# Performance work log

Measured on AMD Instinct MI355X. Metric: run time of the kernel, lower is better.

The kernel has to match this reference:

```python
import jax, jax.numpy as jnp
import numpy as np

S, B, H = 1024, 8, 1024   # seq (num_tokens//WORLD_SIZE), batch, hidden
T = S * B                 # total tokens
E, K, F = 8, 2, 4096      # experts, top_k, ffn hidden (4*H)


def setup_inputs() -> dict:
    key = jax.random.key(0)
    k0, k1, k2, k3, k4 = jax.random.split(key, 5)
    hidden_states = jax.random.normal(k0, (S, B, H), dtype=jnp.float32)
    # precomputed top-k router probs (normalized like softmax top-k output)
    gw = jax.random.uniform(k1, (T, K), dtype=jnp.float32) + 1e-3
    gate_weight = gw / jnp.sum(gw, axis=-1, keepdims=True)
    choosed_experts = jax.random.randint(k2, (T, K), 0, E).astype(jnp.int64)
    w1 = jax.random.normal(k3, (E, H, F), dtype=jnp.float32) * 0.02
    w2 = jax.random.normal(k4, (E, F, H), dtype=jnp.float32) * 0.02
    return {"hidden_states": hidden_states, "gate_weight": gate_weight,
            "choosed_experts": choosed_experts, "w1": w1, "w2": w2}


def reference(hidden_states, gate_weight, choosed_experts, w1, w2):
    # Megatron MoE with precomputed routing: dispatch tokens to top-k experts,
    # per-expert MLP (fc1 -> gelu -> fc2, no bias), combine weighted by probs.
    x = hidden_states.reshape(-1, H)  # [T, H]
    n_exp = w1.shape[0]
    # coef[t, e] = sum_k gate_weight[t, k] * 1[choosed_experts[t, k] == e]
    onehot = jax.nn.one_hot(choosed_experts, n_exp, dtype=gate_weight.dtype)  # [T, K, E]
    coef = jnp.einsum('tk,tke->te', gate_weight, onehot)  # [T, E]
    out = jnp.zeros_like(x)
    for e in range(n_exp):  # fixed small loop over experts (grouped GEMM)
        h = jax.nn.gelu(x @ w1[e])          # [T, F]
        out = out + coef[:, e:e + 1] * (h @ w2[e])  # [T, H]
    output = out.reshape(-1, H)
    return output  # mlp_bias is None in grouped-GEMM Megatron experts
```

## Files before the change

### kernel.cpp

```cpp
#include <hip/hip_runtime.h>
#include <stdint.h>

#define T 8192
#define H 1024
#define F 4096
#define E 8
#define K_TOP 2
#define TK (T * K_TOP)

#define BM 128
#define BN 128
#define BK 32

typedef unsigned short u16;
typedef __bf16 bf16x8 __attribute__((ext_vector_type(8)));
typedef float f32x4 __attribute__((ext_vector_type(4)));

__device__ __forceinline__ u16 f2bf(float f) {
    union { float f; uint32_t u; } v; v.f = f;
    uint32_t r = v.u + 0x7FFFu + ((v.u >> 16) & 1u);
    return (u16)(r >> 16);
}

__device__ __forceinline__ void async_cp16(const u16* g, u16* l) {
    __builtin_amdgcn_global_load_lds(
        (const __attribute__((address_space(1))) void*)g,
        (__attribute__((address_space(3))) void*)l, 16, 0, 0);
}

__global__ __launch_bounds__(256) void count_kernel(const int* __restrict__ ce,
                                                    int* __restrict__ counts) {
    int p = blockIdx.x * 256 + threadIdx.x;
    if (p < TK) atomicAdd(&counts[ce[p]], 1);
}

__global__ void scan_kernel(const int* __restrict__ counts, int* __restrict__ offsets) {
    if (threadIdx.x == 0) {
        int s = 0;
        for (int e = 0; e < E; e++) { offsets[e] = s; s += counts[e]; }
    }
}

__global__ __launch_bounds__(256) void fill_kernel(const int* __restrict__ ce,
                                                   const float* __restrict__ gate,
                                                   const int* __restrict__ offsets,
                                                   int* __restrict__ fill,
                                                   int* __restrict__ tokbuf,
                                                   float* __restrict__ gwbuf) {
    int p = blockIdx.x * 256 + threadIdx.x;
    if (p < TK) {
        int e = ce[p];
        int pos = offsets[e] + atomicAdd(&fill[e], 1);
        tokbuf[pos] = p >> 1;
        gwbuf[pos] = gate[p];
    }
}

__global__ __launch_bounds__(256) void cvt_bf16(const float* __restrict__ in,
                                                u16* __restrict__ out, int n) {
    int i = (blockIdx.x * 256 + threadIdx.x) * 4;
    if (i < n) {
        float4 v = *(const float4*)(in + i);
        ushort4 o;
        o.x = f2bf(v.x); o.y = f2bf(v.y); o.z = f2bf(v.z); o.w = f2bf(v.w);
        *(ushort4*)(out + i) = o;
    }
}

__global__ __launch_bounds__(256) void transpose_cvt(const float* __restrict__ in,
                                                     u16* __restrict__ out,
                                                     int R, int C) {
    __shared__ u16 tile[64][66];
    int e = blockIdx.z;
    const float* src = in + (size_t)e * R * C;
    u16* dst = out + (size_t)e * R * C;
    int c0 = blockIdx.x * 64, r0 = blockIdx.y * 64;
    int tx = threadIdx.x & 63, ty = threadIdx.x >> 6;
#pragma unroll
    for (int p = 0; p < 16; p++) {
        int row = ty + p * 4;
        tile[row][tx] = f2bf(src[(size_t)(r0 + row) * C + c0 + tx]);
    }
    __syncthreads();
#pragma unroll
    for (int p = 0; p < 16; p++) {
        int row = ty + p * 4;
        dst[(size_t)(c0 + row) * R + r0 + tx] = tile[tx][row];
    }
}

__global__ __launch_bounds__(256, 2) void fc1_kernel(const u16* __restrict__ xb,
                                                     const u16* __restrict__ w1t,
                                                     const int* __restrict__ tokbuf,
                                                     const int* __restrict__ counts,
                                                     const int* __restrict__ offsets,
                                                     u16* __restrict__ hbuf) {
    __shared__ __align__(16) u16 As[BM * BK];
    __shared__ __align__(16) u16 Bs[BN * BK];

    const int e = blockIdx.z;
    const int cnt = counts[e];
    const int off = offsets[e];
    const int nt = blockIdx.x;
    const int tid = threadIdx.x;
    const int lane = tid & 63;
    const int wave = tid >> 6;
    const int wr = wave >> 1, wc = wave & 1;
    const int quad = lane >> 4, l16 = lane & 15;
    const int r0 = tid >> 2;
    const int kc = tid & 3;

    for (int rt = blockIdx.y; rt * BM < cnt; rt += gridDim.y) {
        int m0 = rt * BM + r0, m1 = m0 + 64;
        int t0 = tokbuf[off + (m0 < cnt ? m0 : cnt - 1)];
        int t1 = tokbuf[off + (m1 < cnt ? m1 : cnt - 1)];
        const u16* a0 = xb + (size_t)t0 * H + kc * 8;
        const u16* a1 = xb + (size_t)t1 * H + kc * 8;
        const u16* b0 = w1t + ((size_t)e * F + nt * BN + r0) * H + kc * 8;
        const u16* b1 = b0 + (size_t)64 * H;

        f32x4 acc[4][4];
#pragma unroll
        for (int i = 0; i < 4; i++)
#pragma unroll
            for (int j = 0; j < 4; j++) acc[i][j] = (f32x4)0.f;

        for (int k0 = 0; k0 < H; k0 += BK) {
            __syncthreads();
            async_cp16(a0 + k0, &As[tid * 8]);
            async_cp16(a1 + k0, &As[(tid + 256) * 8]);
            async_cp16(b0 + k0, &Bs[tid * 8]);
            async_cp16(b1 + k0, &Bs[(tid + 256) * 8]);
            __syncthreads();

            bf16x8 af[4], bfv[4];
#pragma unroll
            for (int mi = 0; mi < 4; mi++)
                af[mi] = *(const bf16x8*)&As[(wr * 64 + mi * 16 + l16) * BK + quad * 8];
#pragma unroll
            for (int ni = 0; ni < 4; ni++)
                bfv[ni] = *(const bf16x8*)&Bs[(wc * 64 + ni * 16 + l16) * BK + quad * 8];
#pragma unroll
            for (int mi = 0; mi < 4; mi++)
#pragma unroll
                for (int ni = 0; ni < 4; ni++)
                    acc[mi][ni] = __builtin_amdgcn_mfma_f32_16x16x32_bf16(
                        af[mi], bfv[ni], acc[mi][ni], 0, 0, 0);
        }

#pragma unroll
        for (int mi = 0; mi < 4; mi++) {
#pragma unroll
            for (int r = 0; r < 4; r++) {
                int m = rt * BM + wr * 64 + mi * 16 + quad * 4 + r;
                if (m < cnt) {
                    size_t rowbase = (size_t)(off + m) * F;
#pragma unroll
                    for (int ni = 0; ni < 4; ni++) {
                        float v = acc[mi][ni][r];
                        float u = 0.7978845608028654f * (v + 0.044715f * v * v * v);
                        float g = v / (1.f + __expf(-2.f * u));
                        int fcol = nt * BN + wc * 64 + ni * 16 + l16;
                        hbuf[rowbase + fcol] = f2bf(g);
                    }
                }
            }
        }
    }
}

__global__ __launch_bounds__(256, 2) void fc2_kernel(const u16* __restrict__ hbuf,
                                                     const u16* __restrict__ w2t,
                                                     const int* __restrict__ tokbuf,
                                                     const float* __restrict__ gwbuf,
                                                     const int* __restrict__ counts,
                                                     const int* __restrict__ offsets,
                                                     float* __restrict__ out) {
    __shared__ __align__(16) u16 As[BM * BK];
    __shared__ __align__(16) u16 Bs[BN * BK];

    const int e = blockIdx.z;
    const int cnt = counts[e];
    const int off = offsets[e];
    const int nt = blockIdx.x;
    const int tid = threadIdx.x;
    const int lane = tid & 63;
    const int wave = tid >> 6;
    const int wr = wave >> 1, wc = wave & 1;
    const int quad = lane >> 4, l16 = lane & 15;
    const int r0 = tid >> 2;
    const int kc = tid & 3;

    for (int rt = blockIdx.y; rt * BM < cnt; rt += gridDim.y) {
        int m0 = rt * BM + r0, m1 = m0 + 64;
        int s0 = off + (m0 < cnt ? m0 : cnt - 1);
        int s1 = off + (m1 < cnt ? m1 : cnt - 1);
        const u16* a0 = hbuf + (size_t)s0 * F + kc * 8;
        const u16* a1 = hbuf + (size_t)s1 * F + kc * 8;
        const u16* b0 = w2t + ((size_t)e * H + nt * BN + r0) * F + kc * 8;
        const u16* b1 = b0 + (size_t)64 * F;

        f32x4 acc[4][4];
#pragma unroll
        for (int i = 0; i < 4; i++)
#pragma unroll
            for (int j = 0; j < 4; j++) acc[i][j] = (f32x4)0.f;

        for (int k0 = 0; k0 < F; k0 += BK) {
            __syncthreads();
            async_cp16(a0 + k0, &As[tid * 8]);
            async_cp16(a1 + k0, &As[(tid + 256) * 8]);
            async_cp16(b0 + k0, &Bs[tid * 8]);
            async_cp16(b1 + k0, &Bs[(tid + 256) * 8]);
            __syncthreads();

            bf16x8 af[4], bfv[4];
#pragma unroll
            for (int mi = 0; mi < 4; mi++)
                af[mi] = *(const bf16x8*)&As[(wr * 64 + mi * 16 + l16) * BK + quad * 8];
#pragma unroll
            for (int ni = 0; ni < 4; ni++)
                bfv[ni] = *(const bf16x8*)&Bs[(wc * 64 + ni * 16 + l16) * BK + quad * 8];
#pragma unroll
            for (int mi = 0; mi < 4; mi++)
#pragma unroll
                for (int ni = 0; ni < 4; ni++)
                    acc[mi][ni] = __builtin_amdgcn_mfma_f32_16x16x32_bf16(
                        af[mi], bfv[ni], acc[mi][ni], 0, 0, 0);
        }

#pragma unroll
        for (int mi = 0; mi < 4; mi++) {
#pragma unroll
            for (int r = 0; r < 4; r++) {
                int m = rt * BM + wr * 64 + mi * 16 + quad * 4 + r;
                if (m < cnt) {
                    int t = tokbuf[off + m];
                    float g = gwbuf[off + m];
                    size_t obase = (size_t)t * H;
#pragma unroll
                    for (int ni = 0; ni < 4; ni++) {
                        int col = nt * BN + wc * 64 + ni * 16 + l16;
                        atomicAdd(&out[obase + col], g * acc[mi][ni][r]);
                    }
                }
            }
        }
    }
}

extern "C" void kernel_launch(void* const* d_in, const int* in_sizes, int n_in,
                              void* d_out, int out_size, void* d_ws, size_t ws_size,
                              hipStream_t stream) {
    const float* x    = (const float*)d_in[0];
    const float* gate = (const float*)d_in[1];
    const int*   ce   = (const int*)d_in[2];
    const float* w1   = (const float*)d_in[3];
    const float* w2   = (const float*)d_in[4];
    float* out = (float*)d_out;
    char* ws = (char*)d_ws;

    int*   counts  = (int*)(ws + 0);
    int*   fill    = (int*)(ws + 32);
    int*   offsets = (int*)(ws + 64);
    int*   tokbuf  = (int*)(ws + 256);
    float* gwbuf   = (float*)(ws + 256 + TK * 4);
    size_t o = 256 + (size_t)TK * 8;
    u16* xb  = (u16*)(ws + o);  o += (size_t)T * H * 2;
    u16* w1t = (u16*)(ws + o);  o += (size_t)E * F * H * 2;
    u16* w2t = (u16*)(ws + o);  o += (size_t)E * H * F * 2;
    u16* hbuf = (u16*)(ws + o);

    hipMemsetAsync(ws, 0, 256, stream);
    hipMemsetAsync(d_out, 0, (size_t)T * H * sizeof(float), stream);

    count_kernel<<<TK / 256, 256, 0, stream>>>(ce, counts);
    scan_kernel<<<1, 64, 0, stream>>>(counts, offsets);
    fill_kernel<<<TK / 256, 256, 0, stream>>>(ce, gate, offsets, fill, tokbuf, gwbuf);

    cvt_bf16<<<(T * H) / (256 * 4), 256, 0, stream>>>(x, xb, T * H);
    transpose_cvt<<<dim3(F / 64, H / 64, E), 256, 0, stream>>>(w1, w1t, H, F);
    transpose_cvt<<<dim3(H / 64, F / 64, E), 256, 0, stream>>>(w2, w2t, F, H);

    fc1_kernel<<<dim3(F / BN, 32, E), 256, 0, stream>>>(xb, w1t, tokbuf, counts, offsets, hbuf);
    fc2_kernel<<<dim3(H / BN, 32, E), 256, 0, stream>>>(hbuf, w2t, tokbuf, gwbuf, counts, offsets, out);
}
```

Before: 934.3 us.

## Double-buffer LDS tiles in expert GEMMs and vectorize weight transpose

Both grouped GEMM kernels now keep two LDS buffers per operand and issue the async copy for the next K-slice before running the MFMAs on the current one. This cuts the loop to one barrier per iteration and lets global loads overlap with compute. The weight transpose-convert kernel now reads float4 and writes ushort4 instead of scalars. LDS use per block doubles, which may lower occupancy. Whether the async copy has finished before the single barrier depends on how async_cp16 waits.

```diff
diff --git a/kernel.cpp b/kernel.cpp
--- a/kernel.cpp
+++ b/kernel.cpp
@@ -75,17 +75,27 @@
     const float* src = in + (size_t)e * R * C;
     u16* dst = out + (size_t)e * R * C;
     int c0 = blockIdx.x * 64, r0 = blockIdx.y * 64;
-    int tx = threadIdx.x & 63, ty = threadIdx.x >> 6;
-#pragma unroll
-    for (int p = 0; p < 16; p++) {
-        int row = ty + p * 4;
-        tile[row][tx] = f2bf(src[(size_t)(r0 + row) * C + c0 + tx]);
+    int q = threadIdx.x & 15;
+    int s = threadIdx.x >> 4;
+#pragma unroll
+    for (int p = 0; p < 4; p++) {
+        int row = s + p * 16;
+        float4 v = *(const float4*)(src + (size_t)(r0 + row) * C + c0 + q * 4);
+        tile[row][q * 4 + 0] = f2bf(v.x);
+        tile[row][q * 4 + 1] = f2bf(v.y);
+        tile[row][q * 4 + 2] = f2bf(v.z);
+        tile[row][q * 4 + 3] = f2bf(v.w);
     }
     __syncthreads();
 #pragma unroll
-    for (int p = 0; p < 16; p++) {
-        int row = ty + p * 4;
-        dst[(size_t)(c0 + row) * R + r0 + tx] = tile[tx][row];
+    for (int p = 0; p < 4; p++) {
+        int c = s + p * 16;
+        ushort4 o;
+        o.x = tile[q * 4 + 0][c];
+        o.y = tile[q * 4 + 1][c];
+        o.z = tile[q * 4 + 2][c];
+        o.w = tile[q * 4 + 3][c];
+        *(ushort4*)(dst + (size_t)(c0 + c) * R + r0 + q * 4) = o;
     }
 }
 
@@ -95,8 +105,8 @@
                                                      const int* __restrict__ counts,
                                                      const int* __restrict__ offsets,
                                                      u16* __restrict__ hbuf) {
-    __shared__ __align__(16) u16 As[BM * BK];
-    __shared__ __align__(16) u16 Bs[BN * BK];
+    __shared__ __align__(16) u16 As[2][BM * BK];
+    __shared__ __align__(16) u16 Bs[2][BM * BK];
 
     const int e = blockIdx.z;
     const int cnt = counts[e];
@@ -125,27 +135,38 @@
 #pragma unroll
             for (int j = 0; j < 4; j++) acc[i][j] = (f32x4)0.f;
 
+        async_cp16(a0, &As[0][tid * 8]);
+        async_cp16(a1, &As[0][(tid + 256) * 8]);
+        async_cp16(b0, &Bs[0][tid * 8]);
+        async_cp16(b1, &Bs[0][(tid + 256) * 8]);
+        __syncthreads();
+
+        int cur = 0;
         for (int k0 = 0; k0 < H; k0 += BK) {
-            __syncthreads();
-            async_cp16(a0 + k0, &As[tid * 8]);
-            async_cp16(a1 + k0, &As[(tid + 256) * 8]);
-            async_cp16(b0 + k0, &Bs[tid * 8]);
-            async_cp16(b1 + k0, &Bs[(tid + 256) * 8]);
-            __syncthreads();
+            int kn = k0 + BK;
+            if (kn < H) {
+                async_cp16(a0 + kn, &As[cur ^ 1][tid * 8]);
+                async_cp16(a1 + kn, &As[cur ^ 1][(tid + 256) * 8]);
+                async_cp16(b0 + kn, &Bs[cur ^ 1][tid * 8]);
+                async_cp16(b1 + kn, &Bs[cur ^ 1][(tid + 256) * 8]);
+            }
 
             bf16x8 af[4], bfv[4];
 #pragma unroll
             for (int mi = 0; mi < 4; mi++)
-                af[mi] = *(const bf16x8*)&As[(wr * 64 + mi * 16 + l16) * BK + quad * 8];
+                af[mi] = *(const bf16x8*)&As[cur][(wr * 64 + mi * 16 + l16) * BK + quad * 8];
 #pragma unroll
             for (int ni = 0; ni < 4; ni++)
-                bfv[ni] = *(const bf16x8*)&Bs[(wc * 64 + ni * 16 + l16) * BK + quad * 8];
+                bfv[ni] = *(const bf16x8*)&Bs[cur][(wc * 64 + ni * 16 + l16) * BK + quad * 8];
 #pragma unroll
             for (int mi = 0; mi < 4; mi++)
 #pragma unroll
                 for (int ni = 0; ni < 4; ni++)
                     acc[mi][ni] = __builtin_amdgcn_mfma_f32_16x16x32_bf16(
                         af[mi], bfv[ni], acc[mi][ni], 0, 0, 0);
+
+            __syncthreads();
+            cur ^= 1;
         }
 
 #pragma unroll
@@ -176,8 +197,8 @@
                                                      const int* __restrict__ counts,
                                                      const int* __restrict__ offsets,
                                                      float* __restrict__ out) {
-    __shared__ __align__(16) u16 As[BM * BK];
-    __shared__ __align__(16) u16 Bs[BN * BK];
+    __shared__ __align__(16) u16 As[2][BM * BK];
+    __shared__ __align__(16) u16 Bs[2][BM * BK];
 
     const int e = blockIdx.z;
     const int cnt = counts[e];
@@ -206,27 +227,38 @@
 #pragma unroll
             for (int j = 0; j < 4; j++) acc[i][j] = (f32x4)0.f;
 
+        async_cp16(a0, &As[0][tid * 8]);
+        async_cp16(a1, &As[0][(tid + 256) * 8]);
+        async_cp16(b0, &Bs[0][tid * 8]);
+        async_cp16(b1, &Bs[0][(tid + 256) * 8]);
+        __syncthreads();
+
+        int cur = 0;
         for (int k0 = 0; k0 < F; k0 += BK) {
-            __syncthreads();
-            async_cp16(a0 + k0, &As[tid * 8]);
-            async_cp16(a1 + k0, &As[(tid + 256) * 8]);
-            async_cp16(b0 + k0, &Bs[tid * 8]);
-            async_cp16(b1 + k0, &Bs[(tid + 256) * 8]);
-            __syncthreads();
+            int kn = k0 + BK;
+            if (kn < F) {
+                async_cp16(a0 + kn, &As[cur ^ 1][tid * 8]);
+                async_cp16(a1 + kn, &As[cur ^ 1][(tid + 256) * 8]);
+                async_cp16(b0 + kn, &Bs[cur ^ 1][tid * 8]);
+                async_cp16(b1 + kn, &Bs[cur ^ 1][(tid + 256) * 8]);
+            }
 
             bf16x8 af[4], bfv[4];
 #pragma unroll
             for (int mi = 0; mi < 4; mi++)
-                af[mi] = *(const bf16x8*)&As[(wr * 64 + mi * 16 + l16) * BK + quad * 8];
+                af[mi] = *(const bf16x8*)&As[cur][(wr * 64 + mi * 16 + l16) * BK + quad * 8];
 #pragma unroll
             for (int ni = 0; ni < 4; ni++)
-                bfv[ni] = *(const bf16x8*)&Bs[(wc * 64 + ni * 16 + l16) * BK + quad * 8];
+                bfv[ni] = *(const bf16x8*)&Bs[cur][(wc * 64 + ni * 16 + l16) * BK + quad * 8];
 #pragma unroll
             for (int mi = 0; mi < 4; mi++)
 #pragma unroll
                 for (int ni = 0; ni < 4; ni++)
                     acc[mi][ni] = __builtin_amdgcn_mfma_f32_16x16x32_bf16(
                         af[mi], bfv[ni], acc[mi][ni], 0, 0, 0);
+
+            __syncthreads();
+            cur ^= 1;
         }
 
 #pragma unroll
```

Measured after the change: 1.056 ms. 13.0% more time.

## Swizzle GEMM block order for XCD locality, halve row grid, vectorize transpose

Applied to the files above, without the earlier changes.

The fc1 and fc2 kernels remap the flat block index so that consecutive blocks, which round-robin across the 8 XCDs, are grouped and share weight tiles within an XCD's L2. The row-tile grid dimension drops from 32 to 16, so each block loops over more row tiles. The weight transpose-convert kernel now uses float4 loads and ushort4 stores instead of scalar accesses. Halving the grid lowers parallelism, and with about 2048 rows per expert the 16 row tiles roughly match the work, but load balance may suffer.

```diff
diff --git a/kernel.cpp b/kernel.cpp
--- a/kernel.cpp
+++ b/kernel.cpp
@@ -75,17 +75,27 @@
     const float* src = in + (size_t)e * R * C;
     u16* dst = out + (size_t)e * R * C;
     int c0 = blockIdx.x * 64, r0 = blockIdx.y * 64;
-    int tx = threadIdx.x & 63, ty = threadIdx.x >> 6;
-#pragma unroll
-    for (int p = 0; p < 16; p++) {
-        int row = ty + p * 4;
-        tile[row][tx] = f2bf(src[(size_t)(r0 + row) * C + c0 + tx]);
+    int q = threadIdx.x & 15;
+    int s = threadIdx.x >> 4;
+#pragma unroll
+    for (int p = 0; p < 4; p++) {
+        int row = s + p * 16;
+        float4 v = *(const float4*)(src + (size_t)(r0 + row) * C + c0 + q * 4);
+        tile[row][q * 4 + 0] = f2bf(v.x);
+        tile[row][q * 4 + 1] = f2bf(v.y);
+        tile[row][q * 4 + 2] = f2bf(v.z);
+        tile[row][q * 4 + 3] = f2bf(v.w);
     }
     __syncthreads();
 #pragma unroll
-    for (int p = 0; p < 16; p++) {
-        int row = ty + p * 4;
-        dst[(size_t)(c0 + row) * R + r0 + tx] = tile[tx][row];
+    for (int p = 0; p < 4; p++) {
+        int c = s + p * 16;
+        ushort4 o;
+        o.x = tile[q * 4 + 0][c];
+        o.y = tile[q * 4 + 1][c];
+        o.z = tile[q * 4 + 2][c];
+        o.w = tile[q * 4 + 3][c];
+        *(ushort4*)(dst + (size_t)(c0 + c) * R + r0 + q * 4) = o;
     }
 }
 
@@ -101,7 +111,11 @@
     const int e = blockIdx.z;
     const int cnt = counts[e];
     const int off = offsets[e];
-    const int nt = blockIdx.x;
+    const int fhw = blockIdx.x + 32 * blockIdx.y;
+    const int f   = (fhw & 7) * 64 + (fhw >> 3);
+    const int nt  = f & 31;
+    const int by  = f >> 5;
+
     const int tid = threadIdx.x;
     const int lane = tid & 63;
     const int wave = tid >> 6;
@@ -110,7 +124,7 @@
     const int r0 = tid >> 2;
     const int kc = tid & 3;
 
-    for (int rt = blockIdx.y; rt * BM < cnt; rt += gridDim.y) {
+    for (int rt = by; rt * BM < cnt; rt += 16) {
         int m0 = rt * BM + r0, m1 = m0 + 64;
         int t0 = tokbuf[off + (m0 < cnt ? m0 : cnt - 1)];
         int t1 = tokbuf[off + (m1 < cnt ? m1 : cnt - 1)];
@@ -182,7 +196,11 @@
     const int e = blockIdx.z;
     const int cnt = counts[e];
     const int off = offsets[e];
-    const int nt = blockIdx.x;
+    const int fhw = blockIdx.x + 8 * blockIdx.y;
+    const int f   = (fhw & 7) * 16 + (fhw >> 3);
+    const int nt  = f & 7;
+    const int by  = f >> 3;
+
     const int tid = threadIdx.x;
     const int lane = tid & 63;
     const int wave = tid >> 6;
@@ -191,7 +209,7 @@
     const int r0 = tid >> 2;
     const int kc = tid & 3;
 
-    for (int rt = blockIdx.y; rt * BM < cnt; rt += gridDim.y) {
+    for (int rt = by; rt * BM < cnt; rt += 16) {
         int m0 = rt * BM + r0, m1 = m0 + 64;
         int s0 = off + (m0 < cnt ? m0 : cnt - 1);
         int s1 = off + (m1 < cnt ? m1 : cnt - 1);
@@ -282,6 +300,6 @@
     transpose_cvt<<<dim3(F / 64, H / 64, E), 256, 0, stream>>>(w1, w1t, H, F);
     transpose_cvt<<<dim3(H / 64, F / 64, E), 256, 0, stream>>>(w2, w2t, F, H);
 
-    fc1_kernel<<<dim3(F / BN, 32, E), 256, 0, stream>>>(xb, w1t, tokbuf, counts, offsets, hbuf);
-    fc2_kernel<<<dim3(H / BN, 32, E), 256, 0, stream>>>(hbuf, w2t, tokbuf, gwbuf, counts, offsets, out);
-}
+    fc1_kernel<<<dim3(F / BN, 16, E), 256, 0, stream>>>(xb, w1t, tokbuf, counts, offsets, hbuf);
+    fc2_kernel<<<dim3(H / BN, 16, E), 256, 0, stream>>>(hbuf, w2t, tokbuf, gwbuf, counts, offsets, out);
+}
```

After: 976.8 us. 1.05x slower.
